# Kernel tuning notes

Hardware: AMD Instinct MI355X
Metric: run time of the kernel (lower is better)

The kernel has to match this reference:

```python
import jax, jax.numpy as jnp
import numpy as np

LEAKAGE = 0.9
RADIUS = 0.1
AVG_DEGREE = 6


def setup_inputs() -> dict:
    key = jax.random.key(0)
    k1, k2, k3, k4, k5 = jax.random.split(key, 5)
    B, T, I, N, O = 16, 2048, 32, 2048, 32
    input_sequence = jax.random.normal(k1, (B, T, I), dtype=jnp.float32)
    # sparse reservoir matrix, uniform(-1,1) with density avg_degree/N, scaled to spectral radius
    A = jax.random.uniform(k2, (N, N), minval=-1.0, maxval=1.0, dtype=jnp.float32)
    mask = jax.random.uniform(k3, (N, N)) < (AVG_DEGREE / N)
    A = jnp.where(mask, A, 0.0)
    # approximate spectral normalization (power-iteration-free surrogate scale)
    A = A * (RADIUS / jnp.max(jnp.abs(jnp.linalg.eigvals(A))).astype(jnp.float32))
    Win = (RADIUS) * (2.0 * jax.random.uniform(k4, (N, I), dtype=jnp.float32) - 1.0)
    Wout_w = jax.random.normal(k5, (O, N), dtype=jnp.float32) / np.sqrt(N)
    return {"input_sequence": input_sequence, "Win": Win, "A": A, "Wout_w": Wout_w, "washout_len": 64}


def reference(input_sequence, Win, A, Wout_w, washout_len):
    # input projection for all timesteps at once (noise_std = 0.0)
    inp = jnp.einsum('bti,ni->btn', input_sequence, Win)  # [B, T, N]
    B = input_sequence.shape[0]
    N = A.shape[0]
    h0 = jnp.zeros((B, N), dtype=input_sequence.dtype)
    At = A.T

    def step(h, u_t):
        # h: [B, N], u_t: [B, N]
        h_new = (1.0 - LEAKAGE) * h + LEAKAGE * jnp.tanh(h @ At + u_t)
        return h_new, h_new

    _, hs = jax.lax.scan(step, h0, jnp.swapaxes(inp, 0, 1))  # hs: [T, B, N]
    hs = jnp.swapaxes(hs, 0, 1)  # [B, T, N]
    h_list = hs[:, washout_len - 1:]  # keep steps i >= washout_len - 1
    return jnp.einsum('btn,on->bto', h_list, Wout_w)
```

## Files before the change

kernel.cpp:

```cpp
#include <hip/hip_runtime.h>
#include <stdint.h>

#define BB 16
#define TT 2048
#define NI 32
#define NN 2048
#define NO 32
#define WASH 64
#define TO (TT - WASH + 1)
#define W 24
#define WT 24
#define CH 16
#define HBST 2056
#define HBROW 4112
#define UROWB 4132
#define U2OFF 65792
#define LDS_BYTES (U2OFF + CH*UROWB)

typedef short bfvec __attribute__((ext_vector_type(8)));
typedef float f4_t  __attribute__((ext_vector_type(4)));

__device__ inline unsigned short f2bf(float f) {
  unsigned int u = __builtin_bit_cast(unsigned int, f);
  unsigned int r = u + 0x7fffu + ((u >> 16) & 1u);
  return (unsigned short)(r >> 16);
}
__device__ inline float bf2f(unsigned short s) {
  unsigned int u = ((unsigned int)s) << 16;
  return __builtin_bit_cast(float, u);
}
__device__ inline float tanh_fast(float x) {
  x = fminf(15.f, fmaxf(-15.f, x));
  float e = __expf(x + x);
  float r = __builtin_amdgcn_rcpf(e + 1.0f);
  return (e - 1.0f) * r;
}

__global__ void build_ell(const float* __restrict__ A, uint32_t* __restrict__ ell,
                          uint32_t* __restrict__ deg) {
  int gw = (int)((blockIdx.x * blockDim.x + threadIdx.x) >> 6);
  int lane = (int)(threadIdx.x & 63);
  if (gw >= NN) return;
  const float* row = A + (size_t)gw * NN;
  int base = 0;
  for (int c = 0; c < NN; c += 64) {
    float v = row[c + lane];
    bool nz = (v != 0.0f);
    unsigned long long mask = __ballot(nz);
    int pre = __popcll(mask & ((1ull << lane) - 1ull));
    if (nz) {
      int idx = base + pre;
      if (idx < W) {
        uint32_t packed = (((uint32_t)f2bf(v)) << 16) | (uint32_t)((c + lane) * 4);
        ell[(size_t)gw * W + idx] = packed;
      }
    }
    base += __popcll(mask);
  }
  int d = base < W ? base : W;
  if (lane == 0) deg[gw] = (uint32_t)d;
  for (int k = d + lane; k < W; k += 64) ell[(size_t)gw * W + k] = 0u;
}

__global__ void sortperm(const uint32_t* __restrict__ deg, uint32_t* __restrict__ perm,
                         uint32_t* __restrict__ invp) {
  __shared__ int dg[NN];
  int tid = (int)threadIdx.x;
  dg[tid] = (int)deg[tid];
  dg[tid + 1024] = (int)deg[tid + 1024];
  __syncthreads();
  for (int r = tid; r < NN; r += 1024) {
    int d = dg[r];
    int rank = 0;
    for (int j = 0; j < NN; ++j) {
      int dj = dg[j];
      rank += (dj < d) || (dj == d && j < r);
    }
    perm[rank] = (uint32_t)r;
    invp[r] = (uint32_t)rank;
  }
}

__global__ void pairsort(const uint32_t* __restrict__ deg, const uint32_t* __restrict__ perm,
                         uint32_t* __restrict__ pairrank, uint32_t* __restrict__ pp) {
  __shared__ int ps[1024];
  int p = (int)threadIdx.x;
  int d0 = (int)deg[perm[p]]; if (d0 > W) d0 = W;
  int d1 = (int)deg[perm[2047 - p]]; if (d1 > W) d1 = W;
  int s = d0 + d1; if (s > WT) s = WT;
  ps[p] = s;
  __syncthreads();
  int rank = 0;
  for (int j = 0; j < 1024; ++j) {
    int sj = ps[j];
    rank += (sj < s) || (sj == s && j < p);
  }
  pairrank[p] = (uint32_t)rank;
  pp[rank] = (uint32_t)p;
}

__device__ inline int rank2pos(int r, const uint32_t* pairrank) {
  return (r < 1024) ? (2 * (int)pairrank[r]) : (2 * (int)pairrank[2047 - r] + 1);
}

__device__ inline int bcnt_get(unsigned long long lo, unsigned long long hi, int b) {
  return (int)(((b < 16) ? (lo >> (4 * b)) : (hi >> (4 * (b - 16)))) & 15ull);
}

__global__ void build_pairs(const uint32_t* __restrict__ ell, const uint32_t* __restrict__ deg,
                            const uint32_t* __restrict__ perm, const uint32_t* __restrict__ invp,
                            const uint32_t* __restrict__ pairrank, const uint32_t* __restrict__ pp,
                            uint32_t* __restrict__ pa, uint32_t* __restrict__ pva,
                            uint32_t* __restrict__ pvb, uint32_t* __restrict__ wavecnt) {
  int blk = (int)blockIdx.x;
  int lane = (int)threadIdx.x;
  int t = blk * 64 + lane;
  int p = (int)pp[t];
  uint32_t a_[WT], u_[WT], w_[WT];
  int cnt = 0;
  {
    int ro = (int)perm[p];
    int d = (int)deg[ro]; if (d > W) d = W;
    for (int k = 0; k < d && cnt < WT; ++k) {
      uint32_t e = ell[(size_t)ro * W + k];
      int pos = rank2pos((int)invp[(e & 0xffffu) >> 2], pairrank);
      a_[cnt] = (uint32_t)(pos * 2);
      u_[cnt] = e & 0xffff0000u;
      w_[cnt] = 0u;
      ++cnt;
    }
    ro = (int)perm[2047 - p];
    d = (int)deg[ro]; if (d > W) d = W;
    for (int k = 0; k < d && cnt < WT; ++k) {
      uint32_t e = ell[(size_t)ro * W + k];
      int pos = rank2pos((int)invp[(e & 0xffffu) >> 2], pairrank);
      a_[cnt] = (uint32_t)(pos * 2);
      u_[cnt] = 0u;
      w_[cnt] = e & 0xffff0000u;
      ++cnt;
    }
  }
  int m = cnt;
  #pragma unroll
  for (int off = 32; off; off >>= 1) m = max(m, __shfl_xor(m, off));
  int S = (m <= 8) ? 8 : (m <= 10) ? 10 : (m <= 12) ? 12 : (m <= 14) ? 14 :
          (m <= 16) ? 16 : (m <= 18) ? 18 : (m <= 20) ? 20 : (m <= 22) ? 22 : 24;
  if (lane == 0) wavecnt[blk] = (uint32_t)S;

  uint32_t sa[WT], su[WT], sw[WT];
  for (int s = 0; s < WT; ++s) {
    sa[s] = ((uint32_t)((lane + s) & 31)) << 2;
    su[s] = 0u; sw[s] = 0u;
  }
  uint32_t used = 0;
  for (int s = 0; s < S; ++s) {
    unsigned long long clo = 0ull, chi = 0ull;
    bool placed = false;
    for (int round = 0; round < 3; ++round) {
      int best = -1, bestc = 999;
      if (!placed) {
        for (int k = 0; k < WT; ++k) {
          if (k >= cnt) break;
          if ((used >> k) & 1u) continue;
          int b = (int)((a_[k] >> 2) & 31u);
          int c = bcnt_get(clo, chi, b);
          if (c < bestc) { bestc = c; best = k; }
        }
      }
      int pb = (best >= 0 && !placed) ? (int)((a_[best] >> 2) & 31u) : 32;
      bool force = (round == 2);
      for (int b = 0; b < 32; ++b) {
        unsigned long long mb = __ballot(pb == b);
        if (!mb) continue;
        int have = bcnt_get(clo, chi, b);
        int cap = 2 - have; if (cap < 0) cap = 0;
        if (pb == b && !placed) {
          int rank = __popcll(mb & ((1ull << (unsigned)lane) - 1ull));
          if (force || rank < cap) {
            placed = true;
            used |= (1u << (unsigned)best);
            sa[s] = a_[best]; su[s] = u_[best]; sw[s] = w_[best];
          }
        }
        int nprop = (int)__popcll(mb);
        int add = force ? nprop : (nprop < cap ? nprop : cap);
        int room = 15 - have; if (add > room) add = room;
        if (add > 0) {
          if (b < 16) clo += ((unsigned long long)add) << (4 * b);
          else        chi += ((unsigned long long)add) << (4 * (b - 16));
        }
      }
    }
    if (!placed) {
      int pick = lane & 31;
      for (int j = 0; j < 32; ++j) {
        int b = (lane + j) & 31;
        if (bcnt_get(clo, chi, b) < 2) { pick = b; break; }
      }
      sa[s] = ((uint32_t)pick) << 2;
    }
  }
  for (int k = 0; k < WT; ++k) {
    pa[(size_t)t * WT + k] = sa[k];
    pva[(size_t)t * WT + k] = su[k];
    pvb[(size_t)t * WT + k] = sw[k];
  }
}

__global__ void build_frags(const float* __restrict__ Win, const float* __restrict__ Wout,
                            const uint32_t* __restrict__ perm, const uint32_t* __restrict__ pp,
                            uint32_t* __restrict__ winf, uint32_t* __restrict__ woutf) {
  int f = (int)(blockIdx.x * blockDim.x + threadIdx.x);
  if (f < 32768) {
    int reg = f & 3, lane = (f >> 2) & 63, ntg = f >> 8;
    int n = (ntg << 4) + (lane & 15);
    int k = ((lane >> 4) << 3) + reg * 2;
    int p = (int)pp[n >> 1];
    int np = (int)perm[(n & 1) ? (2047 - p) : p];
    uint32_t lo = f2bf(Win[(size_t)np * NI + k]);
    uint32_t hi = f2bf(Win[(size_t)np * NI + k + 1]);
    winf[f] = lo | (hi << 16);
  } else {
    int g = f - 32768;
    int reg = g & 3, lane = (g >> 2) & 63, kt = (g >> 8) & 63, ot = g >> 14;
    int o = (ot << 4) + (lane & 15);
    int n = (kt << 5) + ((lane >> 4) << 3) + reg * 2;
    int p = (int)pp[n >> 1];
    int n0 = (int)perm[p];
    int n1 = (int)perm[2047 - p];
    uint32_t lo = f2bf(Wout[(size_t)o * NN + n0]);
    uint32_t hi = f2bf(Wout[(size_t)o * NN + n1]);
    woutf[g] = lo | (hi << 16);
  }
}

#define ENT(K, BASE)                                                                 \
  {                                                                                  \
    float hv = bf2f(*(const unsigned short*)(smem + (BASE) + ea##K));                \
    y0 = __builtin_fmaf(__builtin_bit_cast(float, va##K), hv, y0);                   \
    y1 = __builtin_fmaf(__builtin_bit_cast(float, vb##K), hv, y1);                   \
  }

#define ENTS8(B)  ENT(0,B) ENT(1,B) ENT(2,B) ENT(3,B) ENT(4,B) ENT(5,B) ENT(6,B) ENT(7,B)
#define ENTS10(B) ENTS8(B)  ENT(8,B)  ENT(9,B)
#define ENTS12(B) ENTS10(B) ENT(10,B) ENT(11,B)
#define ENTS14(B) ENTS12(B) ENT(12,B) ENT(13,B)
#define ENTS16(B) ENTS14(B) ENT(14,B) ENT(15,B)
#define ENTS18(B) ENTS16(B) ENT(16,B) ENT(17,B)
#define ENTS20(B) ENTS18(B) ENT(18,B) ENT(19,B)
#define ENTS22(B) ENTS20(B) ENT(20,B) ENT(21,B)
#define ENTS24(B) ENTS22(B) ENT(22,B) ENT(23,B)

#define STEPLOOP(ENTS)                                                               \
  _Pragma("unroll 1")                                                                \
  for (int tt = 0; tt < CH; ++tt) {                                                  \
    const int po = ((tt + CH - 1) & (CH - 1)) * HBROW;                               \
    uint32_t uw = *(const uint32_t*)(smem + u2a + tt * UROWB);                       \
    float y0 = bf2f((unsigned short)(uw & 0xffffu));                                 \
    float y1 = bf2f((unsigned short)(uw >> 16));                                     \
    ENTS(po)                                                                         \
    float hn0 = 0.1f * h0 + 0.9f * tanh_fast(y0);                                    \
    float hn1 = 0.1f * h1 + 0.9f * tanh_fast(y1);                                    \
    *(uint32_t*)(smem + hwa + tt * HBROW) =                                          \
        (uint32_t)f2bf(hn0) | ((uint32_t)f2bf(hn1) << 16);                           \
    h0 = hn0; h1 = hn1;                                                              \
    __syncthreads();                                                                 \
  }

__global__ __launch_bounds__(1024, 1) void rec_kernel(
    const float* __restrict__ x,
    const uint32_t* __restrict__ pa, const uint32_t* __restrict__ pva,
    const uint32_t* __restrict__ pvb, const uint32_t* __restrict__ wavecnt,
    const uint32_t* __restrict__ winf, const uint32_t* __restrict__ woutf,
    float* __restrict__ out) {
  extern __shared__ char smem[];
  unsigned short* hb = (unsigned short*)smem;
  float* oscratch = (float*)(smem + U2OFF);

  const int tid = (int)threadIdx.x;
  const int b = (int)blockIdx.x;
  const int lane = tid & 63;
  const int wv = tid >> 6;
  const int la15 = lane & 15;
  const int lg = lane >> 4;
  const int u2a = U2OFF + (tid << 2);
  const int hwa = tid << 2;

  int cnt = __builtin_amdgcn_readfirstlane((int)wavecnt[wv]);

  uint32_t ea0, ea1, ea2, ea3, ea4, ea5, ea6, ea7, ea8, ea9, ea10, ea11,
           ea12, ea13, ea14, ea15, ea16, ea17, ea18, ea19, ea20, ea21, ea22, ea23;
  uint32_t va0, va1, va2, va3, va4, va5, va6, va7, va8, va9, va10, va11,
           va12, va13, va14, va15, va16, va17, va18, va19, va20, va21, va22, va23;
  uint32_t vb0, vb1, vb2, vb3, vb4, vb5, vb6, vb7, vb8, vb9, vb10, vb11,
           vb12, vb13, vb14, vb15, vb16, vb17, vb18, vb19, vb20, vb21, vb22, vb23;
  {
    const uint4* qa = (const uint4*)(pa + (size_t)tid * WT);
    const uint4* qv = (const uint4*)(pva + (size_t)tid * WT);
    const uint4* qw = (const uint4*)(pvb + (size_t)tid * WT);
    uint4 A0 = qa[0], A1 = qa[1], A2 = qa[2], A3 = qa[3], A4 = qa[4], A5 = qa[5];
    uint4 V0 = qv[0], V1 = qv[1], V2 = qv[2], V3 = qv[3], V4 = qv[4], V5 = qv[5];
    uint4 B0 = qw[0], B1 = qw[1], B2 = qw[2], B3 = qw[3], B4 = qw[4], B5 = qw[5];
    ea0 = A0.x; ea1 = A0.y; ea2 = A0.z; ea3 = A0.w;
    ea4 = A1.x; ea5 = A1.y; ea6 = A1.z; ea7 = A1.w;
    ea8 = A2.x; ea9 = A2.y; ea10 = A2.z; ea11 = A2.w;
    ea12 = A3.x; ea13 = A3.y; ea14 = A3.z; ea15 = A3.w;
    ea16 = A4.x; ea17 = A4.y; ea18 = A4.z; ea19 = A4.w;
    ea20 = A5.x; ea21 = A5.y; ea22 = A5.z; ea23 = A5.w;
    va0 = V0.x; va1 = V0.y; va2 = V0.z; va3 = V0.w;
    va4 = V1.x; va5 = V1.y; va6 = V1.z; va7 = V1.w;
    va8 = V2.x; va9 = V2.y; va10 = V2.z; va11 = V2.w;
    va12 = V3.x; va13 = V3.y; va14 = V3.z; va15 = V3.w;
    va16 = V4.x; va17 = V4.y; va18 = V4.z; va19 = V4.w;
    va20 = V5.x; va21 = V5.y; va22 = V5.z; va23 = V5.w;
    vb0 = B0.x; vb1 = B0.y; vb2 = B0.z; vb3 = B0.w;
    vb4 = B1.x; vb5 = B1.y; vb6 = B1.z; vb7 = B1.w;
    vb8 = B2.x; vb9 = B2.y; vb10 = B2.z; vb11 = B2.w;
    vb12 = B3.x; vb13 = B3.y; vb14 = B3.z; vb15 = B3.w;
    vb16 = B4.x; vb17 = B4.y; vb18 = B4.z; vb19 = B4.w;
    vb20 = B5.x; vb21 = B5.y; vb22 = B5.z; vb23 = B5.w;
  }

  *(uint32_t*)(smem + (CH - 1) * HBROW + (tid << 2)) = 0u;
  float h0 = 0.0f, h1 = 0.0f;

  for (int c = 0; c < TT / CH; ++c) {
    const int t0 = c * CH;

    {
      const float* xp = x + ((size_t)b * TT + (t0 + la15)) * NI + (lg << 3);
      float4 x0 = *(const float4*)xp;
      float4 x1 = *(const float4*)(xp + 4);
      union { unsigned short u16[8]; bfvec v; } af;
      af.u16[0]=f2bf(x0.x); af.u16[1]=f2bf(x0.y); af.u16[2]=f2bf(x0.z); af.u16[3]=f2bf(x0.w);
      af.u16[4]=f2bf(x1.x); af.u16[5]=f2bf(x1.y); af.u16[6]=f2bf(x1.z); af.u16[7]=f2bf(x1.w);
      #pragma unroll
      for (int nt = 0; nt < 8; ++nt) {
        int ntg = (wv << 3) + nt;
        union { uint4 q; bfvec v; } bw;
        bw.q = *(const uint4*)(winf + (((size_t)ntg * 64 + lane) << 2));
        f4_t acc = {0.f, 0.f, 0.f, 0.f};
        acc = __builtin_amdgcn_mfma_f32_16x16x32_bf16(bw.v, af.v, acc, 0, 0, 0);
        int dw = (ntg << 3) + (lg << 1);
        uint32_t w0 = (uint32_t)f2bf(acc[0]) | ((uint32_t)f2bf(acc[1]) << 16);
        uint32_t w1 = (uint32_t)f2bf(acc[2]) | ((uint32_t)f2bf(acc[3]) << 16);
        char* ub = smem + U2OFF + la15 * UROWB + (dw << 2);
        *(uint32_t*)(ub) = w0;
        *(uint32_t*)(ub + 4) = w1;
      }
    }
    __syncthreads();

    asm volatile("" : "+s"(cnt));
    if      (cnt <= 8)  { STEPLOOP(ENTS8)  }
    else if (cnt <= 10) { STEPLOOP(ENTS10) }
    else if (cnt <= 12) { STEPLOOP(ENTS12) }
    else if (cnt <= 14) { STEPLOOP(ENTS14) }
    else if (cnt <= 16) { STEPLOOP(ENTS16) }
    else if (cnt <= 18) { STEPLOOP(ENTS18) }
    else if (cnt <= 20) { STEPLOOP(ENTS20) }
    else if (cnt <= 22) { STEPLOOP(ENTS22) }
    else                { STEPLOOP(ENTS24) }

    {
      f4_t oa0 = {0.f,0.f,0.f,0.f}, oa1 = {0.f,0.f,0.f,0.f};
      #pragma unroll
      for (int k4 = 0; k4 < 4; ++k4) {
        int kt = (wv << 2) + k4;
        union { uint4 q; bfvec v; } ha, w0, w1;
        ha.q = *(const uint4*)(hb + (size_t)la15 * HBST + (kt << 5) + (lg << 3));
        w0.q = *(const uint4*)(woutf + (((size_t)(kt) * 64 + lane) << 2));
        w1.q = *(const uint4*)(woutf + (((size_t)(64 + kt) * 64 + lane) << 2));
        oa0 = __builtin_amdgcn_mfma_f32_16x16x32_bf16(ha.v, w0.v, oa0, 0, 0, 0);
        oa1 = __builtin_amdgcn_mfma_f32_16x16x32_bf16(ha.v, w1.v, oa1, 0, 0, 0);
      }
      float* os = oscratch + (wv << 9);
      int tb = lg << 2;
      #pragma unroll
      for (int r = 0; r < 4; ++r) os[(tb + r) * 32 + la15] = oa0[r];
      #pragma unroll
      for (int r = 0; r < 4; ++r) os[(tb + r) * 32 + 16 + la15] = oa1[r];
    }
    __syncthreads();
    if (tid < 512) {
      float s = 0.0f;
      #pragma unroll
      for (int w2 = 0; w2 < 16; ++w2) s += oscratch[(w2 << 9) + tid];
      int tg = t0 + (tid >> 5);
      if (tg >= WASH - 1)
        out[((size_t)b * TO + (tg - (WASH - 1))) * NO + (tid & 31)] = s;
    }
    __syncthreads();
  }
}

extern "C" void kernel_launch(void* const* d_in, const int* in_sizes, int n_in,
                              void* d_out, int out_size, void* d_ws, size_t ws_size,
                              hipStream_t stream) {
  (void)in_sizes; (void)n_in; (void)out_size; (void)ws_size;
  const float* x    = (const float*)d_in[0];
  const float* Win  = (const float*)d_in[1];
  const float* A    = (const float*)d_in[2];
  const float* Wout = (const float*)d_in[3];
  float* out = (float*)d_out;

  char* ws = (char*)d_ws;
  uint32_t* ell      = (uint32_t*)(ws);
  uint32_t* deg      = (uint32_t*)(ws + 196608);
  uint32_t* perm     = (uint32_t*)(ws + 204800);
  uint32_t* invp     = (uint32_t*)(ws + 212992);
  uint32_t* pairrank = (uint32_t*)(ws + 221184);
  uint32_t* pp       = (uint32_t*)(ws + 225280);
  uint32_t* wavecnt  = (uint32_t*)(ws + 229376);
  uint32_t* pa       = (uint32_t*)(ws + 229504);
  uint32_t* pva      = (uint32_t*)(ws + 327808);
  uint32_t* pvb      = (uint32_t*)(ws + 426112);
  uint32_t* winf     = (uint32_t*)(ws + 524416);
  uint32_t* woutf    = (uint32_t*)(ws + 655488);

  hipFuncSetAttribute((const void*)rec_kernel,
                      hipFuncAttributeMaxDynamicSharedMemorySize, 160 * 1024);

  hipLaunchKernelGGL(build_ell, dim3(512), dim3(256), 0, stream, A, ell, deg);
  hipLaunchKernelGGL(sortperm, dim3(1), dim3(1024), 0, stream, deg, perm, invp);
  hipLaunchKernelGGL(pairsort, dim3(1), dim3(1024), 0, stream, deg, perm, pairrank, pp);
  hipLaunchKernelGGL(build_pairs, dim3(16), dim3(64), 0, stream,
                     ell, deg, perm, invp, pairrank, pp, pa, pva, pvb, wavecnt);
  hipLaunchKernelGGL(build_frags, dim3(256), dim3(256), 0, stream, Win, Wout, perm, pp, winf, woutf);
  hipLaunchKernelGGL(rec_kernel, dim3(16), dim3(1024), LDS_BYTES, stream,
                     x, pa, pva, pvb, wavecnt, winf, woutf, out);
}
```

Baseline: 2.798 ms.

## Use exact per-wave slot counts, spread ranking sorts over blocks, improve bank placement

Per-wave slot count S is no longer rounded up to an even bucket, and the recurrent step loop gains specializations for every count from 9 to 23, so each wave runs only the FMA entries it needs every timestep. The bank-conflict-aware slot placement now allows six rounds instead of three and rotates lane priority per slot and round, aiming at fewer LDS bank conflicts in the gathered h loads. The O(N^2) rank sorts are split across several blocks instead of one block of 1024 threads. The cost is more code variants, which grows the instruction footprint, and a slightly longer one-time preprocessing step.

```diff
diff --git a/kernel.cpp b/kernel.cpp
--- a/kernel.cpp
+++ b/kernel.cpp
@@ -66,30 +66,32 @@
                          uint32_t* __restrict__ invp) {
   __shared__ int dg[NN];
   int tid = (int)threadIdx.x;
-  dg[tid] = (int)deg[tid];
-  dg[tid + 1024] = (int)deg[tid + 1024];
+  for (int i = tid; i < NN; i += 256) dg[i] = (int)deg[i];
   __syncthreads();
-  for (int r = tid; r < NN; r += 1024) {
-    int d = dg[r];
-    int rank = 0;
-    for (int j = 0; j < NN; ++j) {
-      int dj = dg[j];
-      rank += (dj < d) || (dj == d && j < r);
-    }
-    perm[rank] = (uint32_t)r;
-    invp[r] = (uint32_t)rank;
-  }
+  int r = (int)blockIdx.x * 256 + tid;
+  int d = dg[r];
+  int rank = 0;
+  for (int j = 0; j < NN; ++j) {
+    int dj = dg[j];
+    rank += (dj < d) || (dj == d && j < r);
+  }
+  perm[rank] = (uint32_t)r;
+  invp[r] = (uint32_t)rank;
 }
 
 __global__ void pairsort(const uint32_t* __restrict__ deg, const uint32_t* __restrict__ perm,
                          uint32_t* __restrict__ pairrank, uint32_t* __restrict__ pp) {
   __shared__ int ps[1024];
-  int p = (int)threadIdx.x;
-  int d0 = (int)deg[perm[p]]; if (d0 > W) d0 = W;
-  int d1 = (int)deg[perm[2047 - p]]; if (d1 > W) d1 = W;
-  int s = d0 + d1; if (s > WT) s = WT;
-  ps[p] = s;
+  int tid = (int)threadIdx.x;
+  for (int i = tid; i < 1024; i += 256) {
+    int d0 = (int)deg[perm[i]]; if (d0 > W) d0 = W;
+    int d1 = (int)deg[perm[2047 - i]]; if (d1 > W) d1 = W;
+    int s = d0 + d1; if (s > WT) s = WT;
+    ps[i] = s;
+  }
   __syncthreads();
+  int p = (int)blockIdx.x * 256 + tid;
+  int s = ps[p];
   int rank = 0;
   for (int j = 0; j < 1024; ++j) {
     int sj = ps[j];
@@ -143,8 +145,7 @@
   int m = cnt;
   #pragma unroll
   for (int off = 32; off; off >>= 1) m = max(m, __shfl_xor(m, off));
-  int S = (m <= 8) ? 8 : (m <= 10) ? 10 : (m <= 12) ? 12 : (m <= 14) ? 14 :
-          (m <= 16) ? 16 : (m <= 18) ? 18 : (m <= 20) ? 20 : (m <= 22) ? 22 : 24;
+  int S = m < 8 ? 8 : (m > 24 ? 24 : m);
   if (lane == 0) wavecnt[blk] = (uint32_t)S;
 
   uint32_t sa[WT], su[WT], sw[WT];
@@ -156,26 +157,29 @@
   for (int s = 0; s < S; ++s) {
     unsigned long long clo = 0ull, chi = 0ull;
     bool placed = false;
-    for (int round = 0; round < 3; ++round) {
+    for (int round = 0; round < 6; ++round) {
+      bool force = (round == 5);
       int best = -1, bestc = 999;
       if (!placed) {
         for (int k = 0; k < WT; ++k) {
           if (k >= cnt) break;
           if ((used >> k) & 1u) continue;
-          int b = (int)((a_[k] >> 2) & 31u);
+        int b = (int)((a_[k] >> 2) & 31u);
           int c = bcnt_get(clo, chi, b);
           if (c < bestc) { bestc = c; best = k; }
         }
       }
-      int pb = (best >= 0 && !placed) ? (int)((a_[best] >> 2) & 31u) : 32;
-      bool force = (round == 2);
+      int pb = (!placed && best >= 0) ? (int)((a_[best] >> 2) & 31u) : 32;
+      int shift = (s * 19 + round * 7) & 63;
+      int mypos = (lane - shift) & 63;
       for (int b = 0; b < 32; ++b) {
         unsigned long long mb = __ballot(pb == b);
         if (!mb) continue;
+        unsigned long long mbr = (mb >> shift) | (mb << ((64 - shift) & 63));
         int have = bcnt_get(clo, chi, b);
         int cap = 2 - have; if (cap < 0) cap = 0;
-        if (pb == b && !placed) {
-          int rank = __popcll(mb & ((1ull << (unsigned)lane) - 1ull));
+        if (pb == b) {
+          int rank = (int)__popcll(mbr & ((1ull << (unsigned)mypos) - 1ull));
           if (force || rank < cap) {
             placed = true;
             used |= (1u << (unsigned)best);
@@ -242,14 +246,22 @@
   }
 
 #define ENTS8(B)  ENT(0,B) ENT(1,B) ENT(2,B) ENT(3,B) ENT(4,B) ENT(5,B) ENT(6,B) ENT(7,B)
-#define ENTS10(B) ENTS8(B)  ENT(8,B)  ENT(9,B)
-#define ENTS12(B) ENTS10(B) ENT(10,B) ENT(11,B)
-#define ENTS14(B) ENTS12(B) ENT(12,B) ENT(13,B)
-#define ENTS16(B) ENTS14(B) ENT(14,B) ENT(15,B)
-#define ENTS18(B) ENTS16(B) ENT(16,B) ENT(17,B)
-#define ENTS20(B) ENTS18(B) ENT(18,B) ENT(19,B)
-#define ENTS22(B) ENTS20(B) ENT(20,B) ENT(21,B)
-#define ENTS24(B) ENTS22(B) ENT(22,B) ENT(23,B)
+#define ENTS9(B)  ENTS8(B)  ENT(8,B)
+#define ENTS10(B) ENTS9(B)  ENT(9,B)
+#define ENTS11(B) ENTS10(B) ENT(10,B)
+#define ENTS12(B) ENTS11(B) ENT(11,B)
+#define ENTS13(B) ENTS12(B) ENT(12,B)
+#define ENTS14(B) ENTS13(B) ENT(13,B)
+#define ENTS15(B) ENTS14(B) ENT(14,B)
+#define ENTS16(B) ENTS15(B) ENT(15,B)
+#define ENTS17(B) ENTS16(B) ENT(16,B)
+#define ENTS18(B) ENTS17(B) ENT(17,B)
+#define ENTS19(B) ENTS18(B) ENT(18,B)
+#define ENTS20(B) ENTS19(B) ENT(19,B)
+#define ENTS21(B) ENTS20(B) ENT(20,B)
+#define ENTS22(B) ENTS21(B) ENT(21,B)
+#define ENTS23(B) ENTS22(B) ENT(22,B)
+#define ENTS24(B) ENTS23(B) ENT(23,B)
 
 #define STEPLOOP(ENTS)                                                               \
   _Pragma("unroll 1")                                                                \
@@ -353,13 +365,21 @@
 
     asm volatile("" : "+s"(cnt));
     if      (cnt <= 8)  { STEPLOOP(ENTS8)  }
-    else if (cnt <= 10) { STEPLOOP(ENTS10) }
-    else if (cnt <= 12) { STEPLOOP(ENTS12) }
-    else if (cnt <= 14) { STEPLOOP(ENTS14) }
-    else if (cnt <= 16) { STEPLOOP(ENTS16) }
-    else if (cnt <= 18) { STEPLOOP(ENTS18) }
-    else if (cnt <= 20) { STEPLOOP(ENTS20) }
-    else if (cnt <= 22) { STEPLOOP(ENTS22) }
+    else if (cnt == 9)  { STEPLOOP(ENTS9)  }
+    else if (cnt == 10) { STEPLOOP(ENTS10) }
+    else if (cnt == 11) { STEPLOOP(ENTS11) }
+    else if (cnt == 12) { STEPLOOP(ENTS12) }
+    else if (cnt == 13) { STEPLOOP(ENTS13) }
+    else if (cnt == 14) { STEPLOOP(ENTS14) }
+    else if (cnt == 15) { STEPLOOP(ENTS15) }
+    else if (cnt == 16) { STEPLOOP(ENTS16) }
+    else if (cnt == 17) { STEPLOOP(ENTS17) }
+    else if (cnt == 18) { STEPLOOP(ENTS18) }
+    else if (cnt == 19) { STEPLOOP(ENTS19) }
+    else if (cnt == 20) { STEPLOOP(ENTS20) }
+    else if (cnt == 21) { STEPLOOP(ENTS21) }
+    else if (cnt == 22) { STEPLOOP(ENTS22) }
+    else if (cnt == 23) { STEPLOOP(ENTS23) }
     else                { STEPLOOP(ENTS24) }
 
     {
@@ -422,8 +442,8 @@
                       hipFuncAttributeMaxDynamicSharedMemorySize, 160 * 1024);
 
   hipLaunchKernelGGL(build_ell, dim3(512), dim3(256), 0, stream, A, ell, deg);
-  hipLaunchKernelGGL(sortperm, dim3(1), dim3(1024), 0, stream, deg, perm, invp);
-  hipLaunchKernelGGL(pairsort, dim3(1), dim3(1024), 0, stream, deg, perm, pairrank, pp);
+  hipLaunchKernelGGL(sortperm, dim3(8), dim3(256), 0, stream, deg, perm, invp);
+  hipLaunchKernelGGL(pairsort, dim3(4), dim3(256), 0, stream, deg, perm, pairrank, pp);
   hipLaunchKernelGGL(build_pairs, dim3(16), dim3(64), 0, stream,
                      ell, deg, perm, invp, pairrank, pp, pa, pva, pvb, wavecnt);
   hipLaunchKernelGGL(build_frags, dim3(256), dim3(256), 0, stream, Win, Wout, perm, pp, winf, woutf);
```

Measured after the change: 2.858 ms. 2.1% more time.
